# Kernel optimization log

Measured on AMD Instinct MI355X. Metric: run time of the kernel, lower is better.

Reference implementation:

```python
import jax, jax.numpy as jnp
import numpy as np
import math

B, S, D, H = 4, 2048, 1024, 16
HD = D // H
MASKED_BIAS = -10000.0

def setup_inputs() -> dict:
    key = jax.random.key(0)
    k1, k2, k3, k4, k5 = jax.random.split(key, 5)
    scale = 0.02
    return {
        "hidden_states": jax.random.normal(k1, (B, S, D), dtype=jnp.float32),
        "w_attn": jax.random.normal(k2, (D, 3 * D), dtype=jnp.float32) * scale,
        "b_attn": jnp.zeros((3 * D,), dtype=jnp.float32),
        "w_proj": jax.random.normal(k3, (D, D), dtype=jnp.float32) * scale,
        "b_proj": jnp.zeros((D,), dtype=jnp.float32),
    }

def reference(hidden_states, w_attn, b_attn, w_proj, b_proj):
    b, s, d = hidden_states.shape
    qkv = hidden_states @ w_attn + b_attn                      # [B,S,3D]
    q, k, v = jnp.split(qkv, 3, axis=-1)
    # split heads -> [B,H,S,HD]
    def split_heads(x):
        return x.reshape(b, s, H, HD).transpose(0, 2, 1, 3)
    q, k, v = split_heads(q), split_heads(k), split_heads(v)
    scores = jnp.einsum("bhqd,bhkd->bhqk", q, k) / math.sqrt(HD)
    causal = jnp.tril(jnp.ones((s, s), dtype=bool))
    scores = jnp.where(causal[None, None], scores, jnp.float32(MASKED_BIAS))
    probs = jax.nn.softmax(scores, axis=-1)
    ctx = jnp.einsum("bhqk,bhkd->bhqd", probs, v)
    ctx = ctx.transpose(0, 2, 1, 3).reshape(b, s, d)           # merge heads
    return ctx @ w_proj + b_proj
```

## Files before the change

kernel.cpp:

```cpp
#include <hip/hip_runtime.h>

typedef unsigned short u16;
typedef __attribute__((ext_vector_type(8))) short short8;
typedef __attribute__((ext_vector_type(4))) float f32x4;
typedef __attribute__((ext_vector_type(4))) unsigned u32x4;

#define Bq 4
#define Sq 2048
#define Dq 1024
#define Hq 16
#define HDq 64
#define BSq 8192

#define QSCALE 0.18033688011112042f

__device__ __forceinline__ u16 f2bf(float f) {
  unsigned u = __builtin_bit_cast(unsigned, f);
  unsigned r = u + 0x7fffu + ((u >> 16) & 1u);
  return (u16)(r >> 16);
}

__device__ __forceinline__ unsigned pk2(float a, float b) {
  unsigned ua = __builtin_bit_cast(unsigned, a) + 0x8000u;
  unsigned ub = __builtin_bit_cast(unsigned, b) + 0x8000u;
  return __builtin_amdgcn_perm(ub, ua, 0x07060302u);
}

__device__ __forceinline__ void gl_lds16(const u16* g, u16* l) {
  __builtin_amdgcn_global_load_lds((const __attribute__((address_space(1))) unsigned int*)g,
                                   (__attribute__((address_space(3))) unsigned int*)l, 16, 0, 0);
}

__device__ __forceinline__ int kperm(int kk) {
  return ((kk & 0x10) << 1) | ((kk & 0x0C) << 1) | ((kk & 0x20) >> 3) | (kk & 3);
}

__global__ void cvt_kernel(const float* __restrict__ in, u16* __restrict__ out, int n4) {
  int i = blockIdx.x * blockDim.x + threadIdx.x;
  if (i >= n4) return;
  float4 v = reinterpret_cast<const float4*>(in)[i];
  ushort4 o;
  o.x = f2bf(v.x); o.y = f2bf(v.y); o.z = f2bf(v.z); o.w = f2bf(v.w);
  reinterpret_cast<ushort4*>(out)[i] = o;
}

__global__ void transpose_cvt(const float* __restrict__ in, u16* __restrict__ out, int R, int C) {
  __shared__ float tile[32][33];
  int c0 = blockIdx.x * 32, r0 = blockIdx.y * 32;
  for (int i = threadIdx.y; i < 32; i += 8)
    tile[i][threadIdx.x] = in[(size_t)(r0 + i) * C + c0 + threadIdx.x];
  __syncthreads();
  for (int i = threadIdx.y; i < 32; i += 8)
    out[(size_t)(c0 + i) * R + r0 + threadIdx.x] = f2bf(tile[threadIdx.x][i]);
}

template<int EPI>
__global__ __launch_bounds__(256)
void gemm_bt(const u16* __restrict__ A, const u16* __restrict__ Bt,
             const float* __restrict__ bias,
             u16* __restrict__ Qb, u16* __restrict__ Kb, u16* __restrict__ Vt,
             float* __restrict__ Out, int Kdim) {
  __shared__ __align__(16) u16 As[2][128 * 32];
  __shared__ __align__(16) u16 Bs[2][128 * 32];
  int tid = threadIdx.x;
  int lane = tid & 63, wid = tid >> 6;
  int wr = wid >> 1, wc = wid & 1;
  int m0 = blockIdx.y * 128, n0 = blockIdx.x * 128;
  int l15 = lane & 15, g = lane >> 4;
  f32x4 acc[4][4] = {};
  int srow = tid >> 2;
  int scol = (((tid & 3) ^ ((tid >> 3) & 3)) * 8);
  int crd = (g ^ ((l15 >> 1) & 3)) * 8;

  const u16* a0p = &A[(size_t)(m0 + srow) * Kdim + scol];
  const u16* a1p = &A[(size_t)(m0 + 64 + srow) * Kdim + scol];
  const u16* b0p = &Bt[(size_t)(n0 + srow) * Kdim + scol];
  const u16* b1p = &Bt[(size_t)(n0 + 64 + srow) * Kdim + scol];

  gl_lds16(a0p, &As[0][wid * 512]);
  gl_lds16(a1p, &As[0][2048 + wid * 512]);
  gl_lds16(b0p, &Bs[0][wid * 512]);
  gl_lds16(b1p, &Bs[0][2048 + wid * 512]);
  __syncthreads();
  int cur = 0;

  for (int k0 = 0; k0 < Kdim; k0 += 32) {
    if (k0 + 32 < Kdim) {
      gl_lds16(a0p + k0 + 32, &As[cur ^ 1][wid * 512]);
      gl_lds16(a1p + k0 + 32, &As[cur ^ 1][2048 + wid * 512]);
      gl_lds16(b0p + k0 + 32, &Bs[cur ^ 1][wid * 512]);
      gl_lds16(b1p + k0 + 32, &Bs[cur ^ 1][2048 + wid * 512]);
    }
    short8 af[4], bfr[4];
#pragma unroll
    for (int m = 0; m < 4; ++m)
      af[m] = *reinterpret_cast<const short8*>(&As[cur][(wr * 64 + m * 16 + l15) * 32 + crd]);
#pragma unroll
    for (int n = 0; n < 4; ++n)
      bfr[n] = *reinterpret_cast<const short8*>(&Bs[cur][(wc * 64 + n * 16 + l15) * 32 + crd]);
    __builtin_amdgcn_s_setprio(1);
#pragma unroll
    for (int m = 0; m < 4; ++m)
#pragma unroll
      for (int n = 0; n < 4; ++n)
        acc[m][n] = __builtin_amdgcn_mfma_f32_16x16x32_bf16(af[m], bfr[n], acc[m][n], 0, 0, 0);
    __builtin_amdgcn_s_setprio(0);
    __syncthreads();
    cur ^= 1;
  }

  int bb = (m0 + wr * 64) >> 11;
  int sb = (m0 + wr * 64) & 2047;

  if (EPI == 1) {
#pragma unroll
    for (int m = 0; m < 4; ++m)
#pragma unroll
      for (int n = 0; n < 4; ++n) {
        int gcol = n0 + wc * 64 + n * 16 + l15;
        float bv = bias[gcol];
#pragma unroll
        for (int r = 0; r < 4; ++r) {
          int grow = m0 + wr * 64 + m * 16 + g * 4 + r;
          Out[(size_t)grow * 1024 + gcol] = acc[m][n][r] + bv;
        }
      }
  } else if (n0 < 1024) {
#pragma unroll
    for (int n = 0; n < 4; ++n) {
      int col = n0 + wc * 64 + n * 16 + l15;
      int hh = col >> 6, d = col & 63;
      float bv = bias[col];
      u16* qb = &Qb[(((size_t)(bb * 16 + hh) * 2048 + sb) << 6) + d];
#pragma unroll
      for (int m = 0; m < 4; ++m)
#pragma unroll
        for (int r = 0; r < 4; ++r)
          qb[(size_t)(m * 16 + g * 4 + r) << 6] = f2bf((acc[m][n][r] + bv) * QSCALE);
    }
  } else if (n0 < 2048) {
#pragma unroll
    for (int n = 0; n < 4; ++n) {
      int col = n0 - 1024 + wc * 64 + n * 16 + l15;
      int hh = col >> 6, d = col & 63;
      float bv = bias[1024 + col];
      u16* kb = &Kb[(((size_t)(bb * 16 + hh) * 2048 + sb) << 6) + d];
#pragma unroll
      for (int m = 0; m < 4; ++m)
#pragma unroll
        for (int r = 0; r < 4; ++r)
          kb[(size_t)(m * 16 + g * 4 + r) << 6] = f2bf(acc[m][n][r] + bv);
    }
  } else {
#pragma unroll
    for (int n = 0; n < 4; ++n) {
      int cc = n0 - 2048 + wc * 64 + n * 16 + l15;
      int hh = cc >> 6, d = cc & 63;
      float bv = bias[2048 + cc];
      u16* dst = &Vt[((size_t)(bb * 16 + hh) * 64 + d) * 2048 + sb];
      u32x4 lo, hi;
      lo[0] = pk2(acc[0][n][0] + bv, acc[0][n][1] + bv);
      lo[1] = pk2(acc[0][n][2] + bv, acc[0][n][3] + bv);
      lo[2] = pk2(acc[2][n][0] + bv, acc[2][n][1] + bv);
      lo[3] = pk2(acc[2][n][2] + bv, acc[2][n][3] + bv);
      hi[0] = pk2(acc[1][n][0] + bv, acc[1][n][1] + bv);
      hi[1] = pk2(acc[1][n][2] + bv, acc[1][n][3] + bv);
      hi[2] = pk2(acc[3][n][0] + bv, acc[3][n][1] + bv);
      hi[3] = pk2(acc[3][n][2] + bv, acc[3][n][3] + bv);
      *reinterpret_cast<u32x4*>(dst + g * 8) = lo;
      *reinterpret_cast<u32x4*>(dst + 32 + g * 8) = hi;
    }
  }
}

__global__ __launch_bounds__(256, 2)
void attn_kernel(const u16* __restrict__ Qb, const u16* __restrict__ Kb,
                 const u16* __restrict__ Vt, u16* __restrict__ Ctx) {
  __shared__ __align__(16) u16 lds[2][2][8][512];
  int tid = threadIdx.x, lane = tid & 63, w = tid >> 6;
  int l15 = lane & 15, g = lane >> 4;
  int bh = blockIdx.y;
  const u16* Qh = Qb + (size_t)bh * Sq * HDq;
  const u16* Kh = Kb + (size_t)bh * Sq * HDq;
  const u16* Vh = Vt + (size_t)bh * HDq * Sq;
  int b = bh >> 4, h = bh & 15;

  int tileA = 31 - (int)blockIdx.x, tileB = (int)blockIdx.x;
  int nkA = tileA + 1;
  int ntot = nkA + tileB + 1;

  const u16* ksrc = Kh + (size_t)(16 * w + l15) * 64 + 8 * g;
  const u16* vsrc = Vh + (size_t)(16 * w + l15) * Sq + 8 * g;

  int tile = tileA;
  int qbase = tileA * 64 + w * 16;

  short8 qf[2];
  qf[0] = *reinterpret_cast<const short8*>(&Qh[(size_t)(qbase + l15) * 64 + 8 * g]);
  qf[1] = *reinterpret_cast<const short8*>(&Qh[(size_t)(qbase + l15) * 64 + 32 + 8 * g]);

  f32x4 acc[4] = {};
  float m_r = -INFINITY, l_r = 0.f;

  gl_lds16(ksrc,      &lds[0][0][2 * w][0]);
  gl_lds16(ksrc + 32, &lds[0][0][2 * w + 1][0]);
  gl_lds16(vsrc,      &lds[0][1][2 * w][0]);
  gl_lds16(vsrc + 32, &lds[0][1][2 * w + 1][0]);
  __syncthreads();
  int cur = 0;

#pragma unroll 1
  for (int it = 0; it < ntot; ++it) {
    bool lastA = (it == nkA - 1);
    int kb = (it < nkA) ? it : it - nkA;
    int k0 = kb * 64;

    if (it + 1 < ntot) {
      int kb2 = (it + 1 < nkA) ? it + 1 : it + 1 - nkA;
      int nk0 = kb2 * 64;
      gl_lds16(ksrc + (size_t)nk0 * 64,      &lds[cur ^ 1][0][2 * w][0]);
      gl_lds16(ksrc + (size_t)nk0 * 64 + 32, &lds[cur ^ 1][0][2 * w + 1][0]);
      gl_lds16(vsrc + nk0,                   &lds[cur ^ 1][1][2 * w][0]);
      gl_lds16(vsrc + nk0 + 32,              &lds[cur ^ 1][1][2 * w + 1][0]);
    }

    short8 kf[4][2], vbf[4][2];
#pragma unroll
    for (int j = 0; j < 4; ++j) {
      kf[j][0] = *reinterpret_cast<const short8*>(&lds[cur][0][2 * j][lane * 8]);
      kf[j][1] = *reinterpret_cast<const short8*>(&lds[cur][0][2 * j + 1][lane * 8]);
    }
#pragma unroll
    for (int n = 0; n < 4; ++n) {
      vbf[n][0] = *reinterpret_cast<const short8*>(&lds[cur][1][2 * n][lane * 8]);
      vbf[n][1] = *reinterpret_cast<const short8*>(&lds[cur][1][2 * n + 1][lane * 8]);
    }

    f32x4 sj[4];
    __builtin_amdgcn_s_setprio(1);
#pragma unroll
    for (int j = 0; j < 4; ++j) {
      f32x4 z = {};
      z = __builtin_amdgcn_mfma_f32_16x16x32_bf16(kf[j][0], qf[0], z, 0, 0, 0);
      z = __builtin_amdgcn_mfma_f32_16x16x32_bf16(kf[j][1], qf[1], z, 0, 0, 0);
      sj[j] = z;
    }
    __builtin_amdgcn_s_setprio(0);

    if (kb == tile) {
      int q = qbase + l15;
#pragma unroll
      for (int j = 0; j < 4; ++j)
#pragma unroll
        for (int r = 0; r < 4; ++r)
          if (k0 + 16 * j + 4 * g + r > q) sj[j][r] = -1e30f;
    }

    float mx = sj[0][0];
#pragma unroll
    for (int j = 0; j < 4; ++j)
#pragma unroll
      for (int r = 0; r < 4; ++r) mx = fmaxf(mx, sj[j][r]);
    mx = fmaxf(mx, __shfl_xor(mx, 16));
    mx = fmaxf(mx, __shfl_xor(mx, 32));

    float mn = m_r;
    if (!__all(mx - mn <= 8.0f)) {
      float mnew = fmaxf(mn, mx);
      float scn = exp2f(mn - mnew);
      float scr[4];
#pragma unroll
      for (int r = 0; r < 4; ++r) scr[r] = __shfl(scn, 4 * g + r);
#pragma unroll
      for (int n = 0; n < 4; ++n)
#pragma unroll
        for (int r = 0; r < 4; ++r) acc[n][r] *= scr[r];
      l_r *= scn;
      m_r = mnew;
      mn = mnew;
    }

    float p[4][4];
    float rs = 0.f;
#pragma unroll
    for (int j = 0; j < 4; ++j)
#pragma unroll
      for (int r = 0; r < 4; ++r) {
        p[j][r] = exp2f(sj[j][r] - mn);
        rs += p[j][r];
      }
    rs += __shfl_xor(rs, 16);
    rs += __shfl_xor(rs, 32);
    l_r += rs;

    u32x4 w0, w1;
    w0[0] = pk2(p[0][0], p[0][1]); w0[1] = pk2(p[0][2], p[0][3]);
    w0[2] = pk2(p[2][0], p[2][1]); w0[3] = pk2(p[2][2], p[2][3]);
    w1[0] = pk2(p[1][0], p[1][1]); w1[1] = pk2(p[1][2], p[1][3]);
    w1[2] = pk2(p[3][0], p[3][1]); w1[3] = pk2(p[3][2], p[3][3]);
    short8 pa0 = __builtin_bit_cast(short8, w0);
    short8 pa1 = __builtin_bit_cast(short8, w1);
    __builtin_amdgcn_s_setprio(1);
#pragma unroll
    for (int n = 0; n < 4; ++n) {
      acc[n] = __builtin_amdgcn_mfma_f32_16x16x32_bf16(pa0, vbf[n][0], acc[n], 0, 0, 0);
      acc[n] = __builtin_amdgcn_mfma_f32_16x16x32_bf16(pa1, vbf[n][1], acc[n], 0, 0, 0);
    }
    __builtin_amdgcn_s_setprio(0);

    if (lastA) {
      float lf[4];
#pragma unroll
      for (int r = 0; r < 4; ++r) lf[r] = __shfl(l_r, 4 * g + r);
#pragma unroll
      for (int r = 0; r < 4; ++r) {
        float inv = 1.0f / lf[r];
        int row = qbase + 4 * g + r;
        size_t obase = ((size_t)(b * Sq + row)) * Dq + h * 64;
#pragma unroll
        for (int n = 0; n < 4; ++n)
          Ctx[obase + 16 * n + l15] = f2bf(acc[n][r] * inv);
      }
      qbase = tileB * 64 + w * 16;
      tile = tileB;
      qf[0] = *reinterpret_cast<const short8*>(&Qh[(size_t)(qbase + l15) * 64 + 8 * g]);
      qf[1] = *reinterpret_cast<const short8*>(&Qh[(size_t)(qbase + l15) * 64 + 32 + 8 * g]);
#pragma unroll
      for (int n = 0; n < 4; ++n) acc[n] = f32x4{};
      m_r = -INFINITY;
      l_r = 0.f;
    }

    __syncthreads();
    cur ^= 1;
  }

  {
    float lf[4];
#pragma unroll
    for (int r = 0; r < 4; ++r) lf[r] = __shfl(l_r, 4 * g + r);
#pragma unroll
    for (int r = 0; r < 4; ++r) {
      float inv = 1.0f / lf[r];
      int row = qbase + 4 * g + r;
      size_t obase = ((size_t)(b * Sq + row)) * Dq + h * 64;
#pragma unroll
      for (int n = 0; n < 4; ++n)
        Ctx[obase + 16 * n + l15] = f2bf(acc[n][r] * inv);
    }
  }
}

extern "C" void kernel_launch(void* const* d_in, const int* in_sizes, int n_in,
                              void* d_out, int out_size, void* d_ws, size_t ws_size,
                              hipStream_t stream) {
  const float* X  = (const float*)d_in[0];
  const float* Wa = (const float*)d_in[1];
  const float* Ba = (const float*)d_in[2];
  const float* Wp = (const float*)d_in[3];
  const float* Bp = (const float*)d_in[4];
  float* Out = (float*)d_out;

  u16* ws  = (u16*)d_ws;
  u16* Xb  = ws;
  u16* WaT = Xb  + (size_t)BSq * Dq;
  u16* WpT = WaT + (size_t)3 * Dq * Dq;
  u16* Qb  = WpT + (size_t)Dq * Dq;
  u16* Kb  = Qb  + (size_t)Bq * Hq * Sq * HDq;
  u16* Vt  = Kb  + (size_t)Bq * Hq * Sq * HDq;
  u16* Ctx = Vt  + (size_t)Bq * Hq * Sq * HDq;

  cvt_kernel<<<(BSq * Dq / 4 + 255) / 256, 256, 0, stream>>>(X, Xb, BSq * Dq / 4);
  transpose_cvt<<<dim3(3 * Dq / 32, Dq / 32), dim3(32, 8), 0, stream>>>(Wa, WaT, Dq, 3 * Dq);
  transpose_cvt<<<dim3(Dq / 32, Dq / 32), dim3(32, 8), 0, stream>>>(Wp, WpT, Dq, Dq);
  gemm_bt<0><<<dim3(3 * Dq / 128, BSq / 128), 256, 0, stream>>>(Xb, WaT, Ba, Qb, Kb, Vt, nullptr, Dq);
  attn_kernel<<<dim3(16, Bq * Hq), 256, 0, stream>>>(Qb, Kb, Vt, Ctx);
  gemm_bt<1><<<dim3(Dq / 128, BSq / 128), 256, 0, stream>>>(Ctx, WpT, Bp, nullptr, nullptr, nullptr, Out, Dq);
}
```

Before: 200.3 us.

## Compute softmax row sums via MFMA, use hardware bf16 pack, swizzle GEMM tiles

The attention kernel now gets the softmax denominator from two extra MFMAs that multiply P by a ones vector, replacing the per-tile scalar reduction and cross-lane shuffles. It also packs probabilities with the native v_cvt_pk_bf16_f32 instruction, advances the K/V prefetch pointers incrementally, and reduces the row max as a tree. Separately, the GEMM kernels remap block indices with a modulo-8 swizzle, likely to spread neighbouring tiles across XCDs for cache locality. The MFMA sum reads bf16-rounded probabilities, so the denominator is computed at slightly lower precision than before.

```diff
diff --git a/kernel.cpp b/kernel.cpp
--- a/kernel.cpp
+++ b/kernel.cpp
@@ -24,6 +24,12 @@
   unsigned ua = __builtin_bit_cast(unsigned, a) + 0x8000u;
   unsigned ub = __builtin_bit_cast(unsigned, b) + 0x8000u;
   return __builtin_amdgcn_perm(ub, ua, 0x07060302u);
+}
+
+__device__ __forceinline__ unsigned cvtpk(float a, float b) {
+  unsigned r;
+  asm("v_cvt_pk_bf16_f32 %0, %1, %2" : "=v"(r) : "v"(a), "v"(b));
+  return r;
 }
 
 __device__ __forceinline__ void gl_lds16(const u16* g, u16* l) {
@@ -65,7 +71,11 @@
   int tid = threadIdx.x;
   int lane = tid & 63, wid = tid >> 6;
   int wr = wid >> 1, wc = wid & 1;
-  int m0 = blockIdx.y * 128, n0 = blockIdx.x * 128;
+  constexpr int NX = (EPI == 0) ? 24 : 8;
+  constexpr int NWG = NX * 64;
+  int orig = (int)blockIdx.x + NX * (int)blockIdx.y;
+  int swz = (orig & 7) * (NWG >> 3) + (orig >> 3);
+  int m0 = (swz / NX) * 128, n0 = (swz % NX) * 128;
   int l15 = lane & 15, g = lane >> 4;
   f32x4 acc[4][4] = {};
   int srow = tid >> 2;
@@ -191,6 +201,8 @@
 
   const u16* ksrc = Kh + (size_t)(16 * w + l15) * 64 + 8 * g;
   const u16* vsrc = Vh + (size_t)(16 * w + l15) * Sq + 8 * g;
+  const u16* kpre = ksrc + 4096;
+  const u16* vpre = vsrc + 64;
 
   int tile = tileA;
   int qbase = tileA * 64 + w * 16;
@@ -199,8 +211,14 @@
   qf[0] = *reinterpret_cast<const short8*>(&Qh[(size_t)(qbase + l15) * 64 + 8 * g]);
   qf[1] = *reinterpret_cast<const short8*>(&Qh[(size_t)(qbase + l15) * 64 + 32 + 8 * g]);
 
+  u16 onebits = (l15 == 0) ? (u16)0x3F80 : (u16)0;
+  short8 vones;
+#pragma unroll
+  for (int i = 0; i < 8; ++i) vones[i] = (short)onebits;
+
   f32x4 acc[4] = {};
-  float m_r = -INFINITY, l_r = 0.f;
+  f32x4 acc_l = {};
+  float m_r = -INFINITY;
 
   gl_lds16(ksrc,      &lds[0][0][2 * w][0]);
   gl_lds16(ksrc + 32, &lds[0][0][2 * w + 1][0]);
@@ -208,20 +226,20 @@
   gl_lds16(vsrc + 32, &lds[0][1][2 * w + 1][0]);
   __syncthreads();
   int cur = 0;
+  int kb = 0;
 
 #pragma unroll 1
   for (int it = 0; it < ntot; ++it) {
     bool lastA = (it == nkA - 1);
-    int kb = (it < nkA) ? it : it - nkA;
-    int k0 = kb * 64;
+    int k0 = kb << 6;
 
     if (it + 1 < ntot) {
-      int kb2 = (it + 1 < nkA) ? it + 1 : it + 1 - nkA;
-      int nk0 = kb2 * 64;
-      gl_lds16(ksrc + (size_t)nk0 * 64,      &lds[cur ^ 1][0][2 * w][0]);
-      gl_lds16(ksrc + (size_t)nk0 * 64 + 32, &lds[cur ^ 1][0][2 * w + 1][0]);
-      gl_lds16(vsrc + nk0,                   &lds[cur ^ 1][1][2 * w][0]);
-      gl_lds16(vsrc + nk0 + 32,              &lds[cur ^ 1][1][2 * w + 1][0]);
+      gl_lds16(kpre,      &lds[cur ^ 1][0][2 * w][0]);
+      gl_lds16(kpre + 32, &lds[cur ^ 1][0][2 * w + 1][0]);
+      gl_lds16(vpre,      &lds[cur ^ 1][1][2 * w][0]);
+      gl_lds16(vpre + 32, &lds[cur ^ 1][1][2 * w + 1][0]);
+      if (it == nkA - 2) { kpre = ksrc; vpre = vsrc; }
+      else               { kpre += 4096; vpre += 64; }
     }
 
     short8 kf[4][2], vbf[4][2];
@@ -256,11 +274,12 @@
           if (k0 + 16 * j + 4 * g + r > q) sj[j][r] = -1e30f;
     }
 
-    float mx = sj[0][0];
-#pragma unroll
-    for (int j = 0; j < 4; ++j)
-#pragma unroll
-      for (int r = 0; r < 4; ++r) mx = fmaxf(mx, sj[j][r]);
+    float a0 = fmaxf(fmaxf(sj[0][0], sj[0][1]), sj[0][2]);
+    float a1 = fmaxf(fmaxf(sj[0][3], sj[1][0]), sj[1][1]);
+    float a2 = fmaxf(fmaxf(sj[1][2], sj[1][3]), sj[2][0]);
+    float a3 = fmaxf(fmaxf(sj[2][1], sj[2][2]), sj[2][3]);
+    float a4 = fmaxf(fmaxf(sj[3][0], sj[3][1]), sj[3][2]);
+    float mx = fmaxf(fmaxf(fmaxf(a0, a1), a2), fmaxf(fmaxf(a3, a4), sj[3][3]));
     mx = fmaxf(mx, __shfl_xor(mx, 16));
     mx = fmaxf(mx, __shfl_xor(mx, 32));
 
@@ -275,29 +294,24 @@
       for (int n = 0; n < 4; ++n)
 #pragma unroll
         for (int r = 0; r < 4; ++r) acc[n][r] *= scr[r];
-      l_r *= scn;
+#pragma unroll
+      for (int r = 0; r < 4; ++r) acc_l[r] *= scr[r];
       m_r = mnew;
       mn = mnew;
     }
 
     float p[4][4];
-    float rs = 0.f;
 #pragma unroll
     for (int j = 0; j < 4; ++j)
 #pragma unroll
-      for (int r = 0; r < 4; ++r) {
+      for (int r = 0; r < 4; ++r)
         p[j][r] = exp2f(sj[j][r] - mn);
-        rs += p[j][r];
-      }
-    rs += __shfl_xor(rs, 16);
-    rs += __shfl_xor(rs, 32);
-    l_r += rs;
 
     u32x4 w0, w1;
-    w0[0] = pk2(p[0][0], p[0][1]); w0[1] = pk2(p[0][2], p[0][3]);
-    w0[2] = pk2(p[2][0], p[2][1]); w0[3] = pk2(p[2][2], p[2][3]);
-    w1[0] = pk2(p[1][0], p[1][1]); w1[1] = pk2(p[1][2], p[1][3]);
-    w1[2] = pk2(p[3][0], p[3][1]); w1[3] = pk2(p[3][2], p[3][3]);
+    w0[0] = cvtpk(p[0][0], p[0][1]); w0[1] = cvtpk(p[0][2], p[0][3]);
+    w0[2] = cvtpk(p[2][0], p[2][1]); w0[3] = cvtpk(p[2][2], p[2][3]);
+    w1[0] = cvtpk(p[1][0], p[1][1]); w1[1] = cvtpk(p[1][2], p[1][3]);
+    w1[2] = cvtpk(p[3][0], p[3][1]); w1[3] = cvtpk(p[3][2], p[3][3]);
     short8 pa0 = __builtin_bit_cast(short8, w0);
     short8 pa1 = __builtin_bit_cast(short8, w1);
     __builtin_amdgcn_s_setprio(1);
@@ -306,12 +320,15 @@
       acc[n] = __builtin_amdgcn_mfma_f32_16x16x32_bf16(pa0, vbf[n][0], acc[n], 0, 0, 0);
       acc[n] = __builtin_amdgcn_mfma_f32_16x16x32_bf16(pa1, vbf[n][1], acc[n], 0, 0, 0);
     }
+    acc_l = __builtin_amdgcn_mfma_f32_16x16x32_bf16(pa0, vones, acc_l, 0, 0, 0);
+    acc_l = __builtin_amdgcn_mfma_f32_16x16x32_bf16(pa1, vones, acc_l, 0, 0, 0);
     __builtin_amdgcn_s_setprio(0);
 
+    kb++;
     if (lastA) {
       float lf[4];
 #pragma unroll
-      for (int r = 0; r < 4; ++r) lf[r] = __shfl(l_r, 4 * g + r);
+      for (int r = 0; r < 4; ++r) lf[r] = __shfl(acc_l[r], 16 * g);
 #pragma unroll
       for (int r = 0; r < 4; ++r) {
         float inv = 1.0f / lf[r];
@@ -323,12 +340,13 @@
       }
       qbase = tileB * 64 + w * 16;
       tile = tileB;
+      kb = 0;
       qf[0] = *reinterpret_cast<const short8*>(&Qh[(size_t)(qbase + l15) * 64 + 8 * g]);
       qf[1] = *reinterpret_cast<const short8*>(&Qh[(size_t)(qbase + l15) * 64 + 32 + 8 * g]);
 #pragma unroll
       for (int n = 0; n < 4; ++n) acc[n] = f32x4{};
+      acc_l = f32x4{};
       m_r = -INFINITY;
-      l_r = 0.f;
     }
 
     __syncthreads();
@@ -338,7 +356,7 @@
   {
     float lf[4];
 #pragma unroll
-    for (int r = 0; r < 4; ++r) lf[r] = __shfl(l_r, 4 * g + r);
+    for (int r = 0; r < 4; ++r) lf[r] = __shfl(acc_l[r], 16 * g);
 #pragma unroll
     for (int r = 0; r < 4; ++r) {
       float inv = 1.0f / lf[r];
```

Measured after the change: 197.0 us. No clear change (-1.7%).
